# Kernel optimization log

Hardware: AMD Instinct MI355X
Metric: run time of the kernel (lower is better)

The kernel has to match this reference:

```python
import jax, jax.numpy as jnp
import numpy as np

EMB_SIZE = 1024  # scale uses model dim per original code (not head_size)

def setup_inputs() -> dict:
    key = jax.random.key(0)
    k1, k2, k3, k4 = jax.random.split(key, 4)
    B, T, E, H = 4, 4096, 1024, 64
    x = jax.random.normal(k1, (B, T, E), dtype=jnp.float32)
    Wq = jax.random.normal(k2, (E, H), dtype=jnp.float32) * (E ** -0.5)
    Wk = jax.random.normal(k3, (E, H), dtype=jnp.float32) * (E ** -0.5)
    Wv = jax.random.normal(k4, (E, H), dtype=jnp.float32) * (E ** -0.5)
    return {"x": x, "Wq": Wq, "Wk": Wk, "Wv": Wv}

def reference(x, Wq, Wk, Wv):
    B, T, E = x.shape
    q = x @ Wq  # [B,T,H]
    k = x @ Wk
    v = x @ Wv
    scale = E ** -0.5  # original scales by emb_size, not head_size
    scores = jnp.einsum('bth,bsh->bts', q, k) * scale  # [B,T,T]
    causal = jnp.tril(jnp.ones((T, T), dtype=bool))
    scores = jnp.where(causal, scores, -jnp.inf)
    weights = jax.nn.softmax(scores, axis=-1)
    # dropout is identity in eval mode (deterministic baseline)
    return jnp.einsum('bts,bsh->bth', weights, v)
```

## Files before the change

kernel.cpp:

```cpp
#include <hip/hip_runtime.h>
#include <hip/hip_bf16.h>

typedef __bf16 bf16_t;
typedef __bf16 bf16x4 __attribute__((ext_vector_type(4)));
typedef __bf16 bf16x8 __attribute__((ext_vector_type(8)));
typedef float f32x4 __attribute__((ext_vector_type(4)));

#define MFMA16(a, b, c) __builtin_amdgcn_mfma_f32_16x16x32_bf16(a, b, c, 0, 0, 0)

static constexpr float LOG2E = 1.44269504088896340736f;
static constexpr float QSCALE = LOG2E / 32.0f;


template <int CTRL>
__device__ __forceinline__ float dppf(float v) {
    return __builtin_bit_cast(
        float, __builtin_amdgcn_mov_dpp(__builtin_bit_cast(int, v), CTRL, 0xf, 0xf, true));
}
__device__ __forceinline__ float rmax16(float t) {
    t = fmaxf(t, dppf<0xB1>(t));
    t = fmaxf(t, dppf<0x4E>(t));
    t = fmaxf(t, dppf<0x141>(t));
    t = fmaxf(t, dppf<0x140>(t));
    return t;
}
__device__ __forceinline__ float rsum16(float t) {
    t += dppf<0xB1>(t);
    t += dppf<0x4E>(t);
    t += dppf<0x141>(t);
    t += dppf<0x140>(t);
    return t;
}

__global__ __launch_bounds__(256) void transpose_w_kernel(const float* __restrict__ Wq,
                                                          const float* __restrict__ Wk,
                                                          const float* __restrict__ Wv,
                                                          bf16_t* __restrict__ wt) {
    __shared__ float tile[64][68];
    int w = blockIdx.x >> 4;
    int e0 = (blockIdx.x & 15) * 64;
    const float* W = (w == 0) ? Wq : ((w == 1) ? Wk : Wv);
    int t = threadIdx.x;
    int r = t >> 2, q = t & 3;
    const float* src = W + (size_t)(e0 + r) * 64 + q * 16;
#pragma unroll
    for (int jj = 0; jj < 4; ++jj) {
        float4 v = *(const float4*)(src + jj * 4);
        *(float4*)&tile[r][q * 16 + jj * 4] = v;
    }
    __syncthreads();
    bf16_t* dst = wt + (size_t)w * 65536 + (size_t)r * 1024 + e0 + q * 16;
    bf16x8 o0, o1;
#pragma unroll
    for (int jj = 0; jj < 8; ++jj) o0[jj] = (bf16_t)tile[q * 16 + jj][r];
#pragma unroll
    for (int jj = 0; jj < 8; ++jj) o1[jj] = (bf16_t)tile[q * 16 + 8 + jj][r];
    *(bf16x8*)dst = o0;
    *(bf16x8*)(dst + 8) = o1;
}

__global__ __launch_bounds__(256) void proj_kernel(const float* __restrict__ x,
                                                   const bf16_t* __restrict__ wt,
                                                   bf16_t* __restrict__ qs,
                                                   bf16_t* __restrict__ ks,
                                                   bf16_t* __restrict__ vt) {
    __shared__ __align__(16) bf16_t xl[16][1040];
    __shared__ float vred[64][17];
    int t = threadIdx.x;
    int r0 = blockIdx.x * 16;
    {
        int row = t >> 4, cb = (t & 15) * 4;
        const float* xr = x + (size_t)(r0 + row) * 1024 + cb;
#pragma unroll
        for (int i = 0; i < 16; ++i) {
            float4 v = *(const float4*)(xr + i * 64);
            bf16_t* d = &xl[row][cb + i * 64];
            d[0] = (bf16_t)v.x; d[1] = (bf16_t)v.y; d[2] = (bf16_t)v.z; d[3] = (bf16_t)v.w;
        }
    }
    __syncthreads();

    int wave = t >> 6, lane = t & 63;
    int lr = lane & 15, lg = lane >> 4;
    int gc0 = wave * 3;
    const bf16_t* wp0 = wt + ((gc0 + 0) >> 2) * 65536 + (((gc0 + 0) & 3) * 16 + lr) * 1024 + lg * 8;
    const bf16_t* wp1 = wt + ((gc0 + 1) >> 2) * 65536 + (((gc0 + 1) & 3) * 16 + lr) * 1024 + lg * 8;
    const bf16_t* wp2 = wt + ((gc0 + 2) >> 2) * 65536 + (((gc0 + 2) & 3) * 16 + lr) * 1024 + lg * 8;

    f32x4 a0 = {0.f, 0.f, 0.f, 0.f}, a1 = a0, a2 = a0;
#pragma unroll 4
    for (int kk = 0; kk < 32; ++kk) {
        bf16x8 af = *(const bf16x8*)&xl[lr][kk * 32 + lg * 8];
        bf16x8 b0 = *(const bf16x8*)(wp0 + kk * 32);
        bf16x8 b1 = *(const bf16x8*)(wp1 + kk * 32);
        bf16x8 b2 = *(const bf16x8*)(wp2 + kk * 32);
        a0 = MFMA16(af, b0, a0);
        a1 = MFMA16(af, b1, a1);
        a2 = MFMA16(af, b2, a2);
    }

    f32x4 accs[3] = {a0, a1, a2};
#pragma unroll
    for (int c = 0; c < 3; ++c) {
        int gc = gc0 + c;
        int w3 = gc >> 2;
        int h = (gc & 3) * 16 + lr;
#pragma unroll
        for (int r = 0; r < 4; ++r) {
            int rr = r0 + lg * 4 + r;
            float v = accs[c][r];
            if (w3 == 0) {
                qs[(size_t)rr * 64 + h] = (bf16_t)(v * QSCALE);
            } else if (w3 == 1) {
                ks[(size_t)rr * 64 + h] = (bf16_t)v;
            } else {
                vred[(gc - 8) * 16 + lr][lg * 4 + r] = v;
            }
        }
    }
    __syncthreads();
    {
        int h = t >> 2, j4 = (t & 3) * 4;
        int bb = r0 >> 12, t0 = r0 & 4095;
        bf16x4 v4;
#pragma unroll
        for (int jj = 0; jj < 4; ++jj) v4[jj] = (bf16_t)vred[h][j4 + jj];
        *(bf16x4*)(vt + ((size_t)(bb * 64 + h)) * 4096 + t0 + j4) = v4;
    }
}

__global__ __launch_bounds__(256) void attn_kernel(const bf16_t* __restrict__ qs,
                                                   const bf16_t* __restrict__ ks,
                                                   const bf16_t* __restrict__ vt,
                                                   bf16_t* __restrict__ po,
                                                   float* __restrict__ pm,
                                                   float* __restrict__ pls) {
    __shared__ __align__(16) bf16_t kt[2][64 * 64];
    __shared__ __align__(16) bf16_t vtl[2][64 * 64];
    __shared__ __align__(16) bf16_t pl[4][16][80];

    int tid = threadIdx.x;
    int wave = tid >> 6, lane = tid & 63;
    int lr = lane & 15, lg = lane >> 4;

    int bid = blockIdx.x;
    int s = bid & 1;
    int jq = (bid >> 1) & 63;
    int b = bid >> 7;
    int qt = (jq & 1) ? (63 - (jq >> 1)) : (jq >> 1);
    int q0 = qt << 6;
    int nk = qt + 1;
    int lo = (nk * s) >> 1;
    int hi = (nk * (s + 1)) >> 1;
    int ntile = hi - lo;

    int srow = tid >> 3, sc = tid & 7;
    int sw8 = srow & 7;
    int koff0 = srow * 64 + ((sc ^ sw8) * 8);
    int koff1 = (32 + srow) * 64 + ((sc ^ sw8) * 8);
    const bf16_t* kg = ks + ((size_t)b * 4096) * 64;
    const bf16_t* vg = vt + ((size_t)b * 64) * 4096;

    const bf16_t* qb = qs + (size_t)(b * 4096 + q0 + wave * 16 + lr) * 64 + lg * 8;
    bf16x8 qf0 = *(const bf16x8*)qb;
    bf16x8 qf1 = *(const bf16x8*)(qb + 32);

    f32x4 o[4];
    float m[4], l[4];
#pragma unroll
    for (int r = 0; r < 4; ++r) {
        o[r] = (f32x4){0.f, 0.f, 0.f, 0.f};
        m[r] = -INFINITY;
        l[r] = 0.f;
    }

    bf16x8 kr0, kr1, vr0, vr1;
    if (ntile > 0) {
        int kb = lo << 6;
        kr0 = *(const bf16x8*)(kg + (size_t)(kb + srow) * 64 + sc * 8);
        kr1 = *(const bf16x8*)(kg + (size_t)(kb + 32 + srow) * 64 + sc * 8);
        vr0 = *(const bf16x8*)(vg + (size_t)srow * 4096 + kb + sc * 8);
        vr1 = *(const bf16x8*)(vg + (size_t)(32 + srow) * 4096 + kb + sc * 8);
    }

    for (int ti = 0; ti < ntile; ++ti) {
        int cur = ti & 1;
        *(bf16x8*)(&kt[cur][koff0]) = kr0;
        *(bf16x8*)(&kt[cur][koff1]) = kr1;
        *(bf16x8*)(&vtl[cur][koff0]) = vr0;
        *(bf16x8*)(&vtl[cur][koff1]) = vr1;
        __syncthreads();
        if (ti + 1 < ntile) {
            int kb = (lo + ti + 1) << 6;
            kr0 = *(const bf16x8*)(kg + (size_t)(kb + srow) * 64 + sc * 8);
            kr1 = *(const bf16x8*)(kg + (size_t)(kb + 32 + srow) * 64 + sc * 8);
            vr0 = *(const bf16x8*)(vg + (size_t)srow * 4096 + kb + sc * 8);
            vr1 = *(const bf16x8*)(vg + (size_t)(32 + srow) * 4096 + kb + sc * 8);
        }

        int gt = lo + ti;
        int kb = gt << 6;
        const bf16_t* kbuf = kt[cur];
        const bf16_t* vbuf = vtl[cur];

        f32x4 z = {0.f, 0.f, 0.f, 0.f};
        f32x4 sv[4];
#pragma unroll
        for (int g = 0; g < 4; ++g) {
            int krow = g * 16 + lr;
            int sw = krow & 7;
            bf16x8 kf0 = *(const bf16x8*)(kbuf + krow * 64 + ((lg ^ sw) * 8));
            bf16x8 kf1 = *(const bf16x8*)(kbuf + krow * 64 + (((4 | lg) ^ sw) * 8));
            sv[g] = MFMA16(qf0, kf0, z);
            sv[g] = MFMA16(qf1, kf1, sv[g]);
        }

        if (gt == nk - 1) {
#pragma unroll
            for (int r = 0; r < 4; ++r) {
                int qrow = q0 + wave * 16 + lg * 4 + r;
#pragma unroll
                for (int g = 0; g < 4; ++g)
                    if (kb + g * 16 + lr > qrow) sv[g][r] = -INFINITY;
            }
        }

#pragma unroll
        for (int r = 0; r < 4; ++r) {
            float t2 = fmaxf(fmaxf(sv[0][r], sv[1][r]), fmaxf(sv[2][r], sv[3][r]));
            t2 = rmax16(t2);
            float mn = fmaxf(m[r], t2);
            float a = __builtin_amdgcn_exp2f(m[r] - mn);
            float p0 = __builtin_amdgcn_exp2f(sv[0][r] - mn);
            float p1 = __builtin_amdgcn_exp2f(sv[1][r] - mn);
            float p2 = __builtin_amdgcn_exp2f(sv[2][r] - mn);
            float p3 = __builtin_amdgcn_exp2f(sv[3][r] - mn);
            float rs = rsum16((p0 + p1) + (p2 + p3));
            l[r] = l[r] * a + rs;
            m[r] = mn;
            o[0][r] *= a; o[1][r] *= a; o[2][r] *= a; o[3][r] *= a;
            int prow = lg * 4 + r;
            pl[wave][prow][lr] = (bf16_t)p0;
            pl[wave][prow][16 + lr] = (bf16_t)p1;
            pl[wave][prow][32 + lr] = (bf16_t)p2;
            pl[wave][prow][48 + lr] = (bf16_t)p3;
        }

        bf16x8 pa0 = *(const bf16x8*)&pl[wave][lr][lg * 8];
        bf16x8 pa1 = *(const bf16x8*)&pl[wave][lr][32 + lg * 8];
#pragma unroll
        for (int oc = 0; oc < 4; ++oc) {
            int drow = oc * 16 + lr;
            int sw = drow & 7;
            bf16x8 vf0 = *(const bf16x8*)(vbuf + drow * 64 + ((lg ^ sw) * 8));
            bf16x8 vf1 = *(const bf16x8*)(vbuf + drow * 64 + (((4 | lg) ^ sw) * 8));
            o[oc] = MFMA16(pa0, vf0, o[oc]);
            o[oc] = MFMA16(pa1, vf1, o[oc]);
        }
    }

    size_t pblk = ((size_t)((b << 6) + qt) << 1) + s;
    bf16_t* pop = po + pblk * 4096;
#pragma unroll
    for (int r = 0; r < 4; ++r) {
        int row = wave * 16 + lg * 4 + r;
#pragma unroll
        for (int oc = 0; oc < 4; ++oc) pop[row * 64 + oc * 16 + lr] = (bf16_t)o[oc][r];
        if (lr == r) {
            pm[pblk * 64 + row] = m[r];
            pls[pblk * 64 + row] = l[r];
        }
    }
}

__global__ __launch_bounds__(256) void merge_kernel(const bf16_t* __restrict__ po,
                                                    const float* __restrict__ pm,
                                                    const float* __restrict__ pls,
                                                    float* __restrict__ out) {
    int gid = blockIdx.x * 256 + threadIdx.x;
    int row = gid >> 2, cq = gid & 3;
    int b = row >> 12, t = row & 4095;
    int qt = t >> 6, lrow = t & 63;
    int pb = ((b << 6) + qt) << 1;

    float m0 = pm[(size_t)pb * 64 + lrow];
    float m1 = pm[(size_t)(pb + 1) * 64 + lrow];
    float M = fmaxf(m0, m1);
    float w0 = (m0 == -INFINITY) ? 0.f : __builtin_amdgcn_exp2f(m0 - M);
    float w1 = (m1 == -INFINITY) ? 0.f : __builtin_amdgcn_exp2f(m1 - M);
    float L = pls[(size_t)pb * 64 + lrow] * w0 + pls[(size_t)(pb + 1) * 64 + lrow] * w1;
    float rL = 1.0f / L;

    const bf16_t* p0 = po + ((size_t)pb * 64 + lrow) * 64 + cq * 16;
    const bf16_t* p1 = po + ((size_t)(pb + 1) * 64 + lrow) * 64 + cq * 16;
    bf16x8 x0 = *(const bf16x8*)p0, x1 = *(const bf16x8*)(p0 + 8);
    bf16x8 y0 = *(const bf16x8*)p1, y1 = *(const bf16x8*)(p1 + 8);
    float* op = out + (size_t)row * 64 + cq * 16;
#pragma unroll
    for (int j = 0; j < 8; ++j) op[j] = (w0 * (float)x0[j] + w1 * (float)y0[j]) * rL;
#pragma unroll
    for (int j = 0; j < 8; ++j) op[8 + j] = (w0 * (float)x1[j] + w1 * (float)y1[j]) * rL;
}

extern "C" void kernel_launch(void* const* d_in, const int* in_sizes, int n_in,
                              void* d_out, int out_size, void* d_ws, size_t ws_size,
                              hipStream_t stream) {
    const float* x  = (const float*)d_in[0];
    const float* Wq = (const float*)d_in[1];
    const float* Wk = (const float*)d_in[2];
    const float* Wv = (const float*)d_in[3];
    float* out = (float*)d_out;

    char* ws = (char*)d_ws;
    bf16_t* qs = (bf16_t*)(ws);
    bf16_t* ks = (bf16_t*)(ws + (2u << 20));
    bf16_t* vt = (bf16_t*)(ws + (4u << 20));
    bf16_t* wt = (bf16_t*)(ws + (6u << 20));
    bf16_t* po = (bf16_t*)(ws + (8u << 20));
    float*  pm = (float*)(ws + (12u << 20));
    float*  pls = (float*)(ws + (12u << 20) + (128u << 10));

    transpose_w_kernel<<<48, 256, 0, stream>>>(Wq, Wk, Wv, wt);
    proj_kernel<<<1024, 256, 0, stream>>>(x, wt, qs, ks, vt);
    attn_kernel<<<512, 256, 0, stream>>>(qs, ks, vt, po, pm, pls);
    merge_kernel<<<256, 256, 0, stream>>>(po, pm, pls, out);
}
```

Baseline: 191.1 us.

## Split attention KV range four ways and stream x directly in projection

The attention kernel now splits each query tile's causal key range into four partitions instead of two, doubling the grid to 1024 blocks. The merge kernel combines four partial results and the workspace offsets grow to fit them. The projection kernel drops its LDS staging of x and loads fp32 x straight from global memory with one-step register prefetch, converting to bf16 in registers. The trade-off is more partial-output traffic and a heavier merge, in return for better load balance and occupancy across the CUs; the projection also re-reads x from global once per wave.

```diff
diff --git a/kernel.cpp b/kernel.cpp
--- a/kernel.cpp
+++ b/kernel.cpp
@@ -64,39 +64,41 @@
                                                    bf16_t* __restrict__ qs,
                                                    bf16_t* __restrict__ ks,
                                                    bf16_t* __restrict__ vt) {
-    __shared__ __align__(16) bf16_t xl[16][1040];
     __shared__ float vred[64][17];
     int t = threadIdx.x;
-    int r0 = blockIdx.x * 16;
-    {
-        int row = t >> 4, cb = (t & 15) * 4;
-        const float* xr = x + (size_t)(r0 + row) * 1024 + cb;
-#pragma unroll
-        for (int i = 0; i < 16; ++i) {
-            float4 v = *(const float4*)(xr + i * 64);
-            bf16_t* d = &xl[row][cb + i * 64];
-            d[0] = (bf16_t)v.x; d[1] = (bf16_t)v.y; d[2] = (bf16_t)v.z; d[3] = (bf16_t)v.w;
-        }
-    }
-    __syncthreads();
-
     int wave = t >> 6, lane = t & 63;
     int lr = lane & 15, lg = lane >> 4;
+    int r0 = blockIdx.x * 16;
     int gc0 = wave * 3;
+
+    const float* xp = x + (size_t)(r0 + lr) * 1024 + lg * 8;
     const bf16_t* wp0 = wt + ((gc0 + 0) >> 2) * 65536 + (((gc0 + 0) & 3) * 16 + lr) * 1024 + lg * 8;
     const bf16_t* wp1 = wt + ((gc0 + 1) >> 2) * 65536 + (((gc0 + 1) & 3) * 16 + lr) * 1024 + lg * 8;
     const bf16_t* wp2 = wt + ((gc0 + 2) >> 2) * 65536 + (((gc0 + 2) & 3) * 16 + lr) * 1024 + lg * 8;
 
     f32x4 a0 = {0.f, 0.f, 0.f, 0.f}, a1 = a0, a2 = a0;
+
+    float4 xa = *(const float4*)(xp);
+    float4 xb = *(const float4*)(xp + 4);
+    bf16x8 b0 = *(const bf16x8*)(wp0);
+    bf16x8 b1 = *(const bf16x8*)(wp1);
+    bf16x8 b2 = *(const bf16x8*)(wp2);
+
 #pragma unroll 4
     for (int kk = 0; kk < 32; ++kk) {
-        bf16x8 af = *(const bf16x8*)&xl[lr][kk * 32 + lg * 8];
-        bf16x8 b0 = *(const bf16x8*)(wp0 + kk * 32);
-        bf16x8 b1 = *(const bf16x8*)(wp1 + kk * 32);
-        bf16x8 b2 = *(const bf16x8*)(wp2 + kk * 32);
+        int nk = (kk + 1) & 31;
+        float4 nxa = *(const float4*)(xp + nk * 32);
+        float4 nxb = *(const float4*)(xp + nk * 32 + 4);
+        bf16x8 nb0 = *(const bf16x8*)(wp0 + nk * 32);
+        bf16x8 nb1 = *(const bf16x8*)(wp1 + nk * 32);
+        bf16x8 nb2 = *(const bf16x8*)(wp2 + nk * 32);
+        bf16x8 af;
+        af[0] = (bf16_t)xa.x; af[1] = (bf16_t)xa.y; af[2] = (bf16_t)xa.z; af[3] = (bf16_t)xa.w;
+        af[4] = (bf16_t)xb.x; af[5] = (bf16_t)xb.y; af[6] = (bf16_t)xb.z; af[7] = (bf16_t)xb.w;
         a0 = MFMA16(af, b0, a0);
         a1 = MFMA16(af, b1, a1);
         a2 = MFMA16(af, b2, a2);
+        xa = nxa; xb = nxb; b0 = nb0; b1 = nb1; b2 = nb2;
     }
 
     f32x4 accs[3] = {a0, a1, a2};
@@ -144,14 +146,14 @@
     int lr = lane & 15, lg = lane >> 4;
 
     int bid = blockIdx.x;
-    int s = bid & 1;
-    int jq = (bid >> 1) & 63;
-    int b = bid >> 7;
+    int s = bid & 3;
+    int jq = (bid >> 2) & 63;
+    int b = bid >> 8;
     int qt = (jq & 1) ? (63 - (jq >> 1)) : (jq >> 1);
     int q0 = qt << 6;
     int nk = qt + 1;
-    int lo = (nk * s) >> 1;
-    int hi = (nk * (s + 1)) >> 1;
+    int lo = (nk * s) >> 2;
+    int hi = (nk * (s + 1)) >> 2;
     int ntile = hi - lo;
 
     int srow = tid >> 3, sc = tid & 7;
@@ -259,7 +261,7 @@
         }
     }
 
-    size_t pblk = ((size_t)((b << 6) + qt) << 1) + s;
+    size_t pblk = ((size_t)((b << 6) + qt) << 2) + s;
     bf16_t* pop = po + pblk * 4096;
 #pragma unroll
     for (int r = 0; r < 4; ++r) {
@@ -281,25 +283,38 @@
     int row = gid >> 2, cq = gid & 3;
     int b = row >> 12, t = row & 4095;
     int qt = t >> 6, lrow = t & 63;
-    int pb = ((b << 6) + qt) << 1;
-
-    float m0 = pm[(size_t)pb * 64 + lrow];
-    float m1 = pm[(size_t)(pb + 1) * 64 + lrow];
-    float M = fmaxf(m0, m1);
-    float w0 = (m0 == -INFINITY) ? 0.f : __builtin_amdgcn_exp2f(m0 - M);
-    float w1 = (m1 == -INFINITY) ? 0.f : __builtin_amdgcn_exp2f(m1 - M);
-    float L = pls[(size_t)pb * 64 + lrow] * w0 + pls[(size_t)(pb + 1) * 64 + lrow] * w1;
+    int pb = ((b << 6) + qt) << 2;
+
+    float mm[4], w[4];
+    float M = -INFINITY;
+#pragma unroll
+    for (int i = 0; i < 4; ++i) {
+        mm[i] = pm[(size_t)(pb + i) * 64 + lrow];
+        M = fmaxf(M, mm[i]);
+    }
+    float L = 0.f;
+#pragma unroll
+    for (int i = 0; i < 4; ++i) {
+        w[i] = (mm[i] == -INFINITY) ? 0.f : __builtin_amdgcn_exp2f(mm[i] - M);
+        L += pls[(size_t)(pb + i) * 64 + lrow] * w[i];
+    }
     float rL = 1.0f / L;
 
-    const bf16_t* p0 = po + ((size_t)pb * 64 + lrow) * 64 + cq * 16;
-    const bf16_t* p1 = po + ((size_t)(pb + 1) * 64 + lrow) * 64 + cq * 16;
-    bf16x8 x0 = *(const bf16x8*)p0, x1 = *(const bf16x8*)(p0 + 8);
-    bf16x8 y0 = *(const bf16x8*)p1, y1 = *(const bf16x8*)(p1 + 8);
+    float acc[16];
+#pragma unroll
+    for (int j = 0; j < 16; ++j) acc[j] = 0.f;
+#pragma unroll
+    for (int i = 0; i < 4; ++i) {
+        const bf16_t* p = po + ((size_t)(pb + i) * 64 + lrow) * 64 + cq * 16;
+        bf16x8 x0 = *(const bf16x8*)p, x1 = *(const bf16x8*)(p + 8);
+#pragma unroll
+        for (int j = 0; j < 8; ++j) acc[j] += w[i] * (float)x0[j];
+#pragma unroll
+        for (int j = 0; j < 8; ++j) acc[8 + j] += w[i] * (float)x1[j];
+    }
     float* op = out + (size_t)row * 64 + cq * 16;
 #pragma unroll
-    for (int j = 0; j < 8; ++j) op[j] = (w0 * (float)x0[j] + w1 * (float)y0[j]) * rL;
-#pragma unroll
-    for (int j = 0; j < 8; ++j) op[8 + j] = (w0 * (float)x1[j] + w1 * (float)y1[j]) * rL;
+    for (int j = 0; j < 16; ++j) op[j] = acc[j] * rL;
 }
 
 extern "C" void kernel_launch(void* const* d_in, const int* in_sizes, int n_in,
@@ -317,11 +332,11 @@
     bf16_t* vt = (bf16_t*)(ws + (4u << 20));
     bf16_t* wt = (bf16_t*)(ws + (6u << 20));
     bf16_t* po = (bf16_t*)(ws + (8u << 20));
-    float*  pm = (float*)(ws + (12u << 20));
-    float*  pls = (float*)(ws + (12u << 20) + (128u << 10));
+    float*  pm = (float*)(ws + (16u << 20));
+    float*  pls = (float*)(ws + (16u << 20) + (256u << 10));
 
     transpose_w_kernel<<<48, 256, 0, stream>>>(Wq, Wk, Wv, wt);
     proj_kernel<<<1024, 256, 0, stream>>>(x, wt, qs, ks, vt);
-    attn_kernel<<<512, 256, 0, stream>>>(qs, ks, vt, po, pm, pls);
+    attn_kernel<<<1024, 256, 0, stream>>>(qs, ks, vt, po, pm, pls);
     merge_kernel<<<256, 256, 0, stream>>>(po, pm, pls, out);
 }
```

New measurement: 205.9 us. 7.8% more time.
